# Optimization experiments

Hardware: AMD Instinct MI355X
Metric: run time of the kernel (lower is better)

Reference implementation:

```python
import jax, jax.numpy as jnp
import numpy as np

E = 8          # num_experts
TOP_K = 2
CAP_RATIO = 1.2


def setup_inputs() -> dict:
    key = jax.random.key(0)
    k1, k2, k3, k4 = jax.random.split(key, 4)
    B, L, D, H = 2, 2048, 768, 2048
    x = jax.random.normal(k1, (B, L, D), dtype=jnp.float32)
    Wg = jax.random.normal(k2, (D, E), dtype=jnp.float32) * 0.02   # gate: Linear(D, E, bias=False)
    W1 = jax.random.normal(k3, (E, D, 2 * H), dtype=jnp.float32) * 0.02  # fc1 per expert (y | gate halves)
    W2 = jax.random.normal(k4, (E, H, D), dtype=jnp.float32) * 0.02      # fc2 per expert
    return {"x": x, "Wg": Wg, "W1": W1, "W2": W2}


def reference(x, Wg, W1, W2):
    B, L, D = x.shape
    H = W2.shape[1]
    xf = x.reshape(-1, D)                      # [N, D]
    N = xf.shape[0]
    capacity = int(CAP_RATIO * N / E)          # static, matches torch int()

    logits = xf @ Wg                           # [N, E]
    scores, idx = jax.lax.top_k(logits, TOP_K) # [N, K] (descending, like torch.topk)
    weights = jax.nn.softmax(scores, axis=-1)  # [N, K]

    # padded token table: row N is a zero token used for unfilled capacity slots
    xpad = jnp.concatenate([xf, jnp.zeros((1, D), xf.dtype)], axis=0)
    wpad_zero = jnp.zeros((1,), weights.dtype)
    out = jnp.zeros((N, D), x.dtype)

    for k in range(TOP_K):
        ik = idx[:, k]                                         # [N] expert id per token
        onehot = (ik[:, None] == jnp.arange(E)[None, :])       # [N, E]
        pos = jnp.cumsum(onehot, axis=0) - 1                   # rank within expert, ascending token order
        posk = jnp.take_along_axis(pos, ik[:, None], axis=1)[:, 0]  # [N]
        keep = posk < capacity                                 # first-come capacity (== indices[:capacity])

        # dispatch buffer [E, C]: token index per slot, N (pad) where unfilled/dropped
        buf = jnp.full((E, capacity), N, dtype=jnp.int32)
        buf = buf.at[ik, posk].set(jnp.arange(N, dtype=jnp.int32), mode="drop")

        xg = xpad[buf]                                         # [E, C, D]
        h = jnp.einsum("ecd,edh->ech", xg, W1)                 # [E, C, 2H]
        act = h[..., :H] * jax.nn.silu(h[..., H:])             # GatedMLP: y * silu(gate)
        ye = jnp.einsum("ech,ehd->ecd", act, W2)               # [E, C, D]

        wk = jnp.where(keep, weights[:, k], 0.0)               # [N]
        w_buf = jnp.concatenate([wk, wpad_zero])[buf]          # [E, C], 0 on pad slots
        out = out.at[buf.reshape(-1)].add(
            (w_buf[..., None] * ye).reshape(E * capacity, D), mode="drop"
        )

    return out.reshape(B, L, D)
```

## Files before the change

### kernel.cpp

```cpp
#include <hip/hip_runtime.h>


typedef _Float16 half8 __attribute__((ext_vector_type(8)));
typedef _Float16 half4t __attribute__((ext_vector_type(4)));
typedef float f4 __attribute__((ext_vector_type(4)));

#define N_TOK 4096
#define DDIM  768
#define HDIM  2048
#define NEXP  8
#define CAP   614
#define CAPP  640

#define XH_OFF    0L
#define W1T_OFF   6292992L
#define YB_OFF    6292992L
#define W2T_OFF   56624640L
#define ACT_OFF   81790464L
#define EIDX_OFF  123733504L
#define WTS_OFF   123766272L
#define TOKL_OFF  123799040L
#define CNT_OFF   123840000L
#define INV_OFF   123840256L

__device__ __forceinline__ void gld16(const void* g, void* l) {
  __builtin_amdgcn_global_load_lds(
      (const __attribute__((address_space(1))) unsigned int*)g,
      (__attribute__((address_space(3))) unsigned int*)l, 16, 0, 0);
}

__device__ __forceinline__ void cvt2_tile(const float* __restrict__ src,
                                          _Float16* __restrict__ dst,
                                          int R, int C, int e, int r0, int c0,
                                          float* __restrict__ tile) {
  long sb = (long)e * R * C;
  int t = threadIdx.x;
  int rrow = t >> 4, c4 = (t & 15) * 4;
#pragma unroll
  for (int h = 0; h < 2; h++)
#pragma unroll
    for (int i = 0; i < 4; i++) {
      int row = i * 16 + rrow;
      f4 v = *(const f4*)(src + sb + (long)(r0 + row) * C + c0 + h * 64 + c4);
      *(f4*)(&tile[h * 4416 + row * 69 + c4]) = v;
    }
  __syncthreads();
#pragma unroll
  for (int h = 0; h < 2; h++)
#pragma unroll
    for (int s = 0; s < 2; s++) {
      int idx = t + s * 256;
      int c = idx >> 3, ch = idx & 7;
      half8 hv;
#pragma unroll
      for (int j = 0; j < 8; j++) hv[j] = (_Float16)tile[h * 4416 + (ch * 8 + j) * 69 + c];
      *(half8*)(dst + sb + (long)(c0 + h * 64 + c) * R + r0 + ch * 8) = hv;
    }
}

__global__ __launch_bounds__(256) void router_kernel(const float* __restrict__ x,
                                                     const float* __restrict__ Wg,
                                                     _Float16* __restrict__ xh,
                                                     int* __restrict__ eidx,
                                                     float* __restrict__ wts) {
  __shared__ float wgT[NEXP * DDIM];
  int t = threadIdx.x;
  for (int i = t; i < DDIM * NEXP; i += 256) wgT[(i & 7) * DDIM + (i >> 3)] = Wg[i];
  __syncthreads();
  int w = t >> 6, lane = t & 63;
  int tok = blockIdx.x * 4 + w;
  if (tok > N_TOK) return;
  if (tok == N_TOK) {
    half4t zz; zz[0] = zz[1] = zz[2] = zz[3] = (_Float16)0.f;
#pragma unroll
    for (int j = 0; j < 3; j++) *(half4t*)(xh + (long)N_TOK * DDIM + (lane + j * 64) * 4) = zz;
    return;
  }
  const float* xr = x + (long)tok * DDIM;
#pragma unroll
  for (int j = 0; j < 3; j++) {
    f4 v = *(const f4*)(xr + (lane + j * 64) * 4);
    half4t hv;
    hv[0] = (_Float16)v[0]; hv[1] = (_Float16)v[1];
    hv[2] = (_Float16)v[2]; hv[3] = (_Float16)v[3];
    *(half4t*)(xh + (long)tok * DDIM + (lane + j * 64) * 4) = hv;
  }
  float acc[8] = {0.f, 0.f, 0.f, 0.f, 0.f, 0.f, 0.f, 0.f};
#pragma unroll
  for (int i = 0; i < 12; i++) {
    float xv = xr[i * 64 + lane];
#pragma unroll
    for (int e2 = 0; e2 < 8; e2++) acc[e2] += xv * wgT[e2 * DDIM + i * 64 + lane];
  }
#pragma unroll
  for (int e2 = 0; e2 < 8; e2++) {
    float v = acc[e2];
    v += __shfl_xor(v, 32); v += __shfl_xor(v, 16); v += __shfl_xor(v, 8);
    v += __shfl_xor(v, 4);  v += __shfl_xor(v, 2);  v += __shfl_xor(v, 1);
    acc[e2] = v;
  }
  if (lane == 0) {
    float m0 = -1e30f; int i0 = 0;
#pragma unroll
    for (int e2 = 0; e2 < 8; e2++) if (acc[e2] > m0) { m0 = acc[e2]; i0 = e2; }
    float m1 = -1e30f; int i1 = 0;
#pragma unroll
    for (int e2 = 0; e2 < 8; e2++) if (e2 != i0 && acc[e2] > m1) { m1 = acc[e2]; i1 = e2; }
    float tt = __expf(m1 - m0);
    float w0 = 1.f / (1.f + tt);
    eidx[tok * 2 + 0] = i0; eidx[tok * 2 + 1] = i1;
    wts[tok * 2 + 0] = w0;  wts[tok * 2 + 1] = 1.f - w0;
  }
}

__global__ __launch_bounds__(256) void scanCvt_kernel(const int* __restrict__ eidx,
                                                      const float* __restrict__ W1,
                                                      int* __restrict__ toklist,
                                                      int* __restrict__ counts,
                                                      int* __restrict__ inv,
                                                      _Float16* __restrict__ w1t) {
  __shared__ float smem[2 * 4416];
  int b = blockIdx.x;

  if (b < 16) {
    if (threadIdx.x >= 64) return;
    int z = b;
    int k = z >> 3, e = z & 7;
    int lane = threadIdx.x;
    int pre[8];
#pragma unroll
    for (int c = 0; c < 8; c++) pre[c] = eidx[(c * 64 + lane) * 2 + k];
    int base = 0;
#pragma unroll
    for (int c = 0; c < 64; c++) {
      int my = pre[c & 7];
      if (c < 56) pre[c & 7] = eidx[((c + 8) * 64 + lane) * 2 + k];
      int n = c * 64 + lane;
      bool pred = (my == e);
      unsigned long long mask = __ballot(pred);
      if (pred) {
        int pos = base + __popcll(mask & ((1ull << lane) - 1ull));
        if (pos < CAP) {
          toklist[z * CAPP + pos] = n;
          inv[n * 2 + k] = z * CAPP + pos;
        } else {
          inv[n * 2 + k] = -1;
        }
      }
      base += __popcll(mask);
    }
    if (lane == 0) counts[z] = (base < CAP) ? base : CAP;
    return;
  }

  int b2 = b - 16;
  int e = b2 / 384, rem = b2 % 384;
  int cx = rem % 12, cy = rem / 12;
  cvt2_tile(W1, w1t, 768, 4096, e, cx * 64, cy * 128, smem);
}

__global__ __launch_bounds__(256, 2) void gemm1_kernel(const _Float16* __restrict__ xh,
                                                       const _Float16* __restrict__ w1t,
                                                       const float* __restrict__ W2,
                                                       _Float16* __restrict__ w2t,
                                                       const int* __restrict__ toklist,
                                                       const int* __restrict__ counts,
                                                       _Float16* __restrict__ act) {
  __shared__ char smem[49664];

  int i = blockIdx.x;
  if (i >= 1280) {
    int b2 = i - 1280;
    int e = b2 / 192, rem = b2 % 192;
    int cx = rem % 32, cy = rem / 32;
    cvt2_tile(W2, w2t, 2048, 768, e, cx * 64, cy * 128, (float*)smem);
    return;
  }

  _Float16* As = (_Float16*)smem;
  _Float16* Bs = (_Float16*)(smem + 16384);
  int* toks = (int*)(smem + 49152);

  int xcd = i & 7, j = i >> 3;
  int m = j % 5, ii = j / 5;
  int k = ii & 1, n = ii >> 1;
  int e = xcd, z = k * 8 + e;
  int count = counts[z];
  int m0 = m * 128;
  if (m0 >= count) return;
  int n0 = n * 128;

  int t = threadIdx.x;
  if (t < 128) {
    int r = m0 + t;
    toks[t] = (r < count) ? toklist[z * CAPP + r] : N_TOK;
  }
  __syncthreads();

  int lane = t & 63, w = t >> 6;
  int l8 = lane >> 3, u8 = lane & 7;

  const _Float16* ag[4]; _Float16* al[4];
#pragma unroll
  for (int s = 0; s < 4; s++) {
    int row = w * 32 + s * 8 + l8;
    ag[s] = xh + (long)toks[row] * DDIM + ((u8 ^ (row & 7)) * 8);
    al[s] = As + row * 64 + u8 * 8;
  }
  const _Float16* bg[8]; _Float16* bl[8];
#pragma unroll
  for (int s = 0; s < 8; s++) {
    int rb = w * 64 + s * 8 + l8;
    int gr = (rb < 128) ? (n0 + rb) : (2048 + n0 + (rb - 128));
    bg[s] = w1t + ((long)e * 4096 + gr) * DDIM + ((u8 ^ (rb & 7)) * 8);
    bl[s] = Bs + rb * 64 + u8 * 8;
  }

  int q = lane >> 4, m16 = lane & 15;
  int wm = w & 1, wn = w >> 1;

  f4 zero4 = {0.f, 0.f, 0.f, 0.f};
  f4 acc[4][4][2];
#pragma unroll
  for (int rt = 0; rt < 4; rt++)
#pragma unroll
    for (int ct = 0; ct < 4; ct++) { acc[rt][ct][0] = zero4; acc[rt][ct][1] = zero4; }

  for (int kk = 0; kk < DDIM; kk += 64) {
    __syncthreads();
#pragma unroll
    for (int s = 0; s < 4; s++) { gld16(ag[s], al[s]); ag[s] += 64; }
#pragma unroll
    for (int s = 0; s < 8; s++) { gld16(bg[s], bl[s]); bg[s] += 64; }
    __syncthreads();

#pragma unroll
    for (int c = 0; c < 2; c++) {
      half8 af[4], bf[4][2];
#pragma unroll
      for (int rt = 0; rt < 4; rt++) {
        int row = wm * 64 + rt * 16 + m16;
        af[rt] = *(const half8*)(As + row * 64 + (((c * 4 + q) ^ (row & 7)) * 8));
      }
#pragma unroll
      for (int ct = 0; ct < 4; ct++) {
        int cb = wn * 64 + ct * 16 + m16;
        int ph = ((c * 4 + q) ^ (cb & 7)) * 8;
        bf[ct][0] = *(const half8*)(Bs + cb * 64 + ph);
        bf[ct][1] = *(const half8*)(Bs + (128 + cb) * 64 + ph);
      }
#pragma unroll
      for (int rt = 0; rt < 4; rt++)
#pragma unroll
        for (int ct = 0; ct < 4; ct++) {
          acc[rt][ct][0] = __builtin_amdgcn_mfma_f32_16x16x32_f16(af[rt], bf[ct][0], acc[rt][ct][0], 0, 0, 0);
          acc[rt][ct][1] = __builtin_amdgcn_mfma_f32_16x16x32_f16(af[rt], bf[ct][1], acc[rt][ct][1], 0, 0, 0);
        }
    }
  }

  long ab = (long)z * CAPP * HDIM;
#pragma unroll
  for (int rt = 0; rt < 4; rt++)
#pragma unroll
    for (int ct = 0; ct < 4; ct++)
#pragma unroll
      for (int r = 0; r < 4; r++) {
        int row = m0 + wm * 64 + rt * 16 + q * 4 + r;
        int col = n0 + wn * 64 + ct * 16 + m16;
        float h1 = acc[rt][ct][0][r], h2 = acc[rt][ct][1][r];
        float s = h2 / (1.f + __expf(-h2));
        act[ab + (long)row * HDIM + col] = (_Float16)(h1 * s);
      }
}

__global__ __launch_bounds__(256, 3) void gemm2_kernel(const _Float16* __restrict__ act,
                                                       const _Float16* __restrict__ w2t,
                                                       const int* __restrict__ counts,
                                                       float* __restrict__ ybuf) {
  int i = blockIdx.x;
  int xcd = i & 7, j = i >> 3;
  int m = j % 5, t2 = j / 5;
  int k = t2 & 1, n = t2 >> 1;
  int e = xcd, z = k * 8 + e;
  int count = counts[z];
  int m0 = m * 128;
  if (m0 >= count) return;
  int n0 = n * 128;

  __shared__ _Float16 As[128 * 64];
  __shared__ _Float16 Bs[128 * 64];

  int t = threadIdx.x;
  int lane = t & 63, w = t >> 6;
  int l8 = lane >> 3, u8 = lane & 7;

  const _Float16* ag[4]; _Float16* al[4];
#pragma unroll
  for (int s = 0; s < 4; s++) {
    int row = w * 32 + s * 8 + l8;
    ag[s] = act + ((long)z * CAPP + m0 + row) * HDIM + ((u8 ^ (row & 7)) * 8);
    al[s] = As + row * 64 + u8 * 8;
  }
  const _Float16* bg[4]; _Float16* bl[4];
#pragma unroll
  for (int s = 0; s < 4; s++) {
    int rb = w * 32 + s * 8 + l8;
    bg[s] = w2t + ((long)e * DDIM + n0 + rb) * HDIM + ((u8 ^ (rb & 7)) * 8);
    bl[s] = Bs + rb * 64 + u8 * 8;
  }

  int q = lane >> 4, m16 = lane & 15;
  int wm = w & 1, wn = w >> 1;

  f4 zero4 = {0.f, 0.f, 0.f, 0.f};
  f4 acc[4][4];
#pragma unroll
  for (int rt = 0; rt < 4; rt++)
#pragma unroll
    for (int ct = 0; ct < 4; ct++) acc[rt][ct] = zero4;

  for (int kk = 0; kk < HDIM; kk += 64) {
    __syncthreads();
#pragma unroll
    for (int s = 0; s < 4; s++) { gld16(ag[s], al[s]); ag[s] += 64; }
#pragma unroll
    for (int s = 0; s < 4; s++) { gld16(bg[s], bl[s]); bg[s] += 64; }
    __syncthreads();

#pragma unroll
    for (int c = 0; c < 2; c++) {
      half8 af[4], bf[4];
#pragma unroll
      for (int rt = 0; rt < 4; rt++) {
        int row = wm * 64 + rt * 16 + m16;
        af[rt] = *(const half8*)(As + row * 64 + (((c * 4 + q) ^ (row & 7)) * 8));
      }
#pragma unroll
      for (int ct = 0; ct < 4; ct++) {
        int cb = wn * 64 + ct * 16 + m16;
        bf[ct] = *(const half8*)(Bs + cb * 64 + (((c * 4 + q) ^ (cb & 7)) * 8));
      }
#pragma unroll
      for (int rt = 0; rt < 4; rt++)
#pragma unroll
        for (int ct = 0; ct < 4; ct++)
          acc[rt][ct] = __builtin_amdgcn_mfma_f32_16x16x32_f16(af[rt], bf[ct], acc[rt][ct], 0, 0, 0);
    }
  }

#pragma unroll
  for (int rt = 0; rt < 4; rt++)
#pragma unroll
    for (int ct = 0; ct < 4; ct++)
#pragma unroll
      for (int r = 0; r < 4; r++) {
        int lr = wm * 64 + rt * 16 + q * 4 + r;
        int col = n0 + wn * 64 + ct * 16 + m16;
        ybuf[((long)z * CAPP + m0 + lr) * DDIM + col] = acc[rt][ct][r];
      }
}

__global__ __launch_bounds__(256) void gather_kernel(const float* __restrict__ ybuf,
                                                     const int* __restrict__ inv,
                                                     const float* __restrict__ wts,
                                                     float* __restrict__ out) {
  int t = threadIdx.x;
  int w = t >> 6, lane = t & 63;
  int tok = blockIdx.x * 4 + w;
  int s0 = inv[tok * 2 + 0], s1 = inv[tok * 2 + 1];
  float w0 = wts[tok * 2 + 0], w1 = wts[tok * 2 + 1];
  float acc[12];
#pragma unroll
  for (int j = 0; j < 12; j++) acc[j] = 0.f;
  int b = lane * 12;
  if (s0 >= 0) {
    const float* y = ybuf + (long)s0 * DDIM + b;
#pragma unroll
    for (int v = 0; v < 3; v++) {
      f4 qv = *(const f4*)(y + v * 4);
#pragma unroll
      for (int j = 0; j < 4; j++) acc[v * 4 + j] += w0 * qv[j];
    }
  }
  if (s1 >= 0) {
    const float* y = ybuf + (long)s1 * DDIM + b;
#pragma unroll
    for (int v = 0; v < 3; v++) {
      f4 qv = *(const f4*)(y + v * 4);
#pragma unroll
      for (int j = 0; j < 4; j++) acc[v * 4 + j] += w1 * qv[j];
    }
  }
  float* o = out + (long)tok * DDIM + b;
#pragma unroll
  for (int v = 0; v < 3; v++) {
    f4 qv;
#pragma unroll
    for (int j = 0; j < 4; j++) qv[j] = acc[v * 4 + j];
    *(f4*)(o + v * 4) = qv;
  }
}


extern "C" void kernel_launch(void* const* d_in, const int* in_sizes, int n_in,
                              void* d_out, int out_size, void* d_ws, size_t ws_size,
                              hipStream_t stream) {
  const float* x  = (const float*)d_in[0];
  const float* Wg = (const float*)d_in[1];
  const float* W1 = (const float*)d_in[2];
  const float* W2 = (const float*)d_in[3];
  float* out = (float*)d_out;
  char* ws = (char*)d_ws;

  _Float16* xh   = (_Float16*)(ws + XH_OFF);
  _Float16* w1t  = (_Float16*)(ws + W1T_OFF);
  float*    ybuf = (float*)(ws + YB_OFF);
  _Float16* w2t  = (_Float16*)(ws + W2T_OFF);
  _Float16* actb = (_Float16*)(ws + ACT_OFF);
  int* eidx      = (int*)(ws + EIDX_OFF);
  float* wts     = (float*)(ws + WTS_OFF);
  int* toklist   = (int*)(ws + TOKL_OFF);
  int* counts    = (int*)(ws + CNT_OFF);
  int* inv       = (int*)(ws + INV_OFF);

  router_kernel<<<1025, 256, 0, stream>>>(x, Wg, xh, eidx, wts);
  scanCvt_kernel<<<3088, 256, 0, stream>>>(eidx, W1, toklist, counts, inv, w1t);
  gemm1_kernel<<<2816, 256, 0, stream>>>(xh, w1t, W2, w2t, toklist, counts, actb);
  gemm2_kernel<<<480, 256, 0, stream>>>(actb, w2t, counts, ybuf);
  gather_kernel<<<1024, 256, 0, stream>>>(ybuf, inv, wts, out);
}
```

Before: 315.4 us.

## Rebalance weight fp16 conversion across router, scan and gemm1 kernels

```diff
diff --git a/kernel.cpp b/kernel.cpp
--- a/kernel.cpp
+++ b/kernel.cpp
@@ -58,17 +58,34 @@
     }
 }
 
-__global__ __launch_bounds__(256) void router_kernel(const float* __restrict__ x,
-                                                     const float* __restrict__ Wg,
-                                                     _Float16* __restrict__ xh,
-                                                     int* __restrict__ eidx,
-                                                     float* __restrict__ wts) {
-  __shared__ float wgT[NEXP * DDIM];
+__device__ __forceinline__ void cvt_w1_block(const float* __restrict__ W1,
+                                             _Float16* __restrict__ w1t,
+                                             int b2, float* __restrict__ smem) {
+  int e = b2 / 384, rem = b2 % 384;
+  int cx = rem % 12, cy = rem / 12;
+  cvt2_tile(W1, w1t, 768, 4096, e, cx * 64, cy * 128, smem);
+}
+
+__global__ __launch_bounds__(256) void routerCvt_kernel(const float* __restrict__ x,
+                                                        const float* __restrict__ Wg,
+                                                        const float* __restrict__ W1,
+                                                        _Float16* __restrict__ xh,
+                                                        _Float16* __restrict__ w1t,
+                                                        int* __restrict__ eidx,
+                                                        float* __restrict__ wts) {
+  __shared__ float smem[2 * 4416];
+  int b = blockIdx.x;
+
+  if (b >= 1025) {
+    cvt_w1_block(W1, w1t, b - 1025, smem);
+    return;
+  }
+
   int t = threadIdx.x;
-  for (int i = t; i < DDIM * NEXP; i += 256) wgT[(i & 7) * DDIM + (i >> 3)] = Wg[i];
+  for (int i = t; i < DDIM * NEXP; i += 256) smem[(i & 7) * DDIM + (i >> 3)] = Wg[i];
   __syncthreads();
   int w = t >> 6, lane = t & 63;
-  int tok = blockIdx.x * 4 + w;
+  int tok = b * 4 + w;
   if (tok > N_TOK) return;
   if (tok == N_TOK) {
     half4t zz; zz[0] = zz[1] = zz[2] = zz[3] = (_Float16)0.f;
@@ -90,7 +107,7 @@
   for (int i = 0; i < 12; i++) {
     float xv = xr[i * 64 + lane];
 #pragma unroll
-    for (int e2 = 0; e2 < 8; e2++) acc[e2] += xv * wgT[e2 * DDIM + i * 64 + lane];
+    for (int e2 = 0; e2 < 8; e2++) acc[e2] += xv * smem[e2 * DDIM + i * 64 + lane];
   }
 #pragma unroll
   for (int e2 = 0; e2 < 8; e2++) {
@@ -115,10 +132,12 @@
 
 __global__ __launch_bounds__(256) void scanCvt_kernel(const int* __restrict__ eidx,
                                                       const float* __restrict__ W1,
+                                                      const float* __restrict__ W2,
                                                       int* __restrict__ toklist,
                                                       int* __restrict__ counts,
                                                       int* __restrict__ inv,
-                                                      _Float16* __restrict__ w1t) {
+                                                      _Float16* __restrict__ w1t,
+                                                      _Float16* __restrict__ w2t) {
   __shared__ float smem[2 * 4416];
   int b = blockIdx.x;
 
@@ -153,34 +172,29 @@
     return;
   }
 
-  int b2 = b - 16;
-  int e = b2 / 384, rem = b2 % 384;
-  int cx = rem % 12, cy = rem / 12;
-  cvt2_tile(W1, w1t, 768, 4096, e, cx * 64, cy * 128, smem);
+  if (b < 1552) {
+    cvt_w1_block(W1, w1t, 1536 + (b - 16), smem);
+    return;
+  }
+
+  int b2 = b - 1552;
+  int e = b2 / 192, rem = b2 % 192;
+  int cx = rem % 32, cy = rem / 32;
+  cvt2_tile(W2, w2t, 2048, 768, e, cx * 64, cy * 128, smem);
 }
 
 __global__ __launch_bounds__(256, 2) void gemm1_kernel(const _Float16* __restrict__ xh,
                                                        const _Float16* __restrict__ w1t,
-                                                       const float* __restrict__ W2,
-                                                       _Float16* __restrict__ w2t,
                                                        const int* __restrict__ toklist,
                                                        const int* __restrict__ counts,
                                                        _Float16* __restrict__ act) {
   __shared__ char smem[49664];
 
-  int i = blockIdx.x;
-  if (i >= 1280) {
-    int b2 = i - 1280;
-    int e = b2 / 192, rem = b2 % 192;
-    int cx = rem % 32, cy = rem / 32;
-    cvt2_tile(W2, w2t, 2048, 768, e, cx * 64, cy * 128, (float*)smem);
-    return;
-  }
-
   _Float16* As = (_Float16*)smem;
   _Float16* Bs = (_Float16*)(smem + 16384);
   int* toks = (int*)(smem + 49152);
 
+  int i = blockIdx.x;
   int xcd = i & 7, j = i >> 3;
   int m = j % 5, ii = j / 5;
   int k = ii & 1, n = ii >> 1;
@@ -424,9 +438,9 @@
   int* counts    = (int*)(ws + CNT_OFF);
   int* inv       = (int*)(ws + INV_OFF);
 
-  router_kernel<<<1025, 256, 0, stream>>>(x, Wg, xh, eidx, wts);
-  scanCvt_kernel<<<3088, 256, 0, stream>>>(eidx, W1, toklist, counts, inv, w1t);
-  gemm1_kernel<<<2816, 256, 0, stream>>>(xh, w1t, W2, w2t, toklist, counts, actb);
+  routerCvt_kernel<<<2561, 256, 0, stream>>>(x, Wg, W1, xh, w1t, eidx, wts);
+  scanCvt_kernel<<<3088, 256, 0, stream>>>(eidx, W1, W2, toklist, counts, inv, w1t, w2t);
+  gemm1_kernel<<<1280, 256, 0, stream>>>(xh, w1t, toklist, counts, actb);
   gemm2_kernel<<<480, 256, 0, stream>>>(actb, w2t, counts, ybuf);
   gather_kernel<<<1024, 256, 0, stream>>>(ybuf, inv, wts, out);
 }
```

Measured after the change: 320.6 us. No clear change (+1.7%).
